# Performance work log

Measured on AMD Instinct MI355X. Metric: run time of the kernel, lower is better.

Reference implementation:

```python
import jax, jax.numpy as jnp
import numpy as np

N = 100000      # nodes
E = 1600000     # edges (avg degree 16)
F_N, F_E, H = 5, 3, 64
L = 3           # num GCN layers


def setup_inputs() -> dict:
    key = jax.random.key(0)
    ks = jax.random.split(key, 20)
    s = 0.05
    p = lambda k, shape: jax.random.normal(k, shape, jnp.float32) * s
    return {
        "x": jax.random.normal(ks[0], (N, F_N), jnp.float32),
        "edge_index": jax.random.randint(ks[1], (2, E), 0, N, dtype=jnp.int32),
        "edge_attr": jax.random.normal(ks[2], (E, F_E), jnp.float32),
        # node / edge encoders
        "Wn": p(ks[3], (F_N, H)), "bn": jnp.zeros((H,), jnp.float32),
        "We": p(ks[4], (F_E, H)), "be": jnp.zeros((H,), jnp.float32),
        # stacked GCNConv weights [L, H, H] and biases [L, H]
        "Wc": p(ks[5], (L, H, H)), "bc": jnp.zeros((L, H), jnp.float32),
        # demand forecast head
        "Wd1": p(ks[6], (H, H // 2)), "bd1": jnp.zeros((H // 2,), jnp.float32),
        "Wd2": p(ks[7], (H // 2, 1)), "bd2": jnp.zeros((1,), jnp.float32),
        # inventory optimizer head
        "Wi1": p(ks[8], (H, H // 2)), "bi1": jnp.zeros((H // 2,), jnp.float32),
        "Wi2": p(ks[9], (H // 2, 1)), "bi2": jnp.zeros((1,), jnp.float32),
    }


def reference(x, edge_index, edge_attr, Wn, bn, We, be, Wc, bc,
              Wd1, bd1, Wd2, bd2, Wi1, bi1, Wi2, bi2):
    src, dst = edge_index[0], edge_index[1]
    n = x.shape[0]

    h = jax.nn.relu(x @ Wn + bn)                      # [N, H]
    _ea = jax.nn.relu(edge_attr @ We + be)            # encoded edge feats (GCNConv ignores them)

    # GCN symmetric normalization with self-loops: deg[i] = in_degree(i) + 1
    ones_e = jnp.ones(src.shape[0], h.dtype)
    deg = jax.ops.segment_sum(ones_e, dst, num_segments=n) + 1.0
    dinv = jax.lax.rsqrt(deg)                         # [N]
    norm_e = dinv[src] * dinv[dst]                    # [E]
    norm_self = (dinv * dinv)[:, None]                # [N, 1]

    for l in range(Wc.shape[0]):
        hw = h @ Wc[l]                                # [N, H]
        msgs = norm_e[:, None] * hw[src]              # gather + scale, [E, H]
        agg = jax.ops.segment_sum(msgs, dst, num_segments=n) + norm_self * hw
        h = jax.nn.relu(agg + bc[l])

    demand = jax.nn.relu(h @ Wd1 + bd1) @ Wd2 + bd2   # [N, 1]
    inventory = jax.nn.relu(h @ Wi1 + bi1) @ Wi2 + bi2
    return demand, inventory
```

## Files before the change

### kernel.cpp

```cpp
#include <hip/hip_runtime.h>

#define H 64
#define FN 5
#define EPB 4096
#define BSHIFT 8
#define CAP2 4864

typedef _Float16 half4 __attribute__((ext_vector_type(4)));
typedef _Float16 half8 __attribute__((ext_vector_type(8)));
typedef float    float8v __attribute__((ext_vector_type(8)));

__global__ void k_bscatter2(const int* __restrict__ src, const int* __restrict__ dst,
                            int* __restrict__ lofs_t, int* __restrict__ bcounts,
                            int* __restrict__ binned, int nE, int nbB, int nbE) {
    __shared__ int lh[512], lpos[512], lcur[512], tmp[256];
    __shared__ int stage[EPB];
    int t = threadIdx.x;
    int e0 = blockIdx.x * EPB;
    int es[16], ed[16];
    lh[t] = 0; lh[t + 256] = 0;
    __syncthreads();
#pragma unroll
    for (int i = 0; i < 16; ++i) {
        int e = e0 + i * 256 + t;
        bool v = e < nE;
        es[i] = v ? src[e] : 0;
        ed[i] = v ? dst[e] : -1;
        if (v) atomicAdd(&lh[ed[i] >> BSHIFT], 1);
    }
    __syncthreads();
    int a0 = lh[2 * t], a1 = lh[2 * t + 1];
    tmp[t] = a0 + a1;
    __syncthreads();
    for (int s = 1; s < 256; s <<= 1) {
        int a = (t >= s) ? tmp[t - s] : 0;
        __syncthreads();
        tmp[t] += a;
        __syncthreads();
    }
    int ex = tmp[t] - (a0 + a1);
    lpos[2 * t] = ex;
    lpos[2 * t + 1] = ex + a0;
    __syncthreads();
    lcur[t] = lpos[t]; lcur[t + 256] = lpos[t + 256];
    for (int b = t; b <= nbB; b += 256) lofs_t[(size_t)b * nbE + blockIdx.x] = lpos[b];
    for (int b = t; b < nbB; b += 256) if (lh[b]) atomicAdd(&bcounts[b], lh[b]);
    __syncthreads();
#pragma unroll
    for (int i = 0; i < 16; ++i) {
        if (ed[i] >= 0) {
            int b = ed[i] >> BSHIFT;
            int p = atomicAdd(&lcur[b], 1);
            stage[p] = es[i] | ((ed[i] & 255) << 17);
        }
    }
    __syncthreads();
    int total = lpos[nbB];
    for (int j = t; j < total; j += 256) binned[e0 + j] = stage[j];
}

__global__ void k_bscan2(const int* __restrict__ bcounts, int* __restrict__ bbase, int nbB) {
    __shared__ int tmp[512];
    int t = threadIdx.x;
    int v = (t < nbB) ? bcounts[t] : 0;
    tmp[t] = v;
    __syncthreads();
    for (int s = 1; s < 512; s <<= 1) {
        int a = (t >= s) ? tmp[t - s] : 0;
        __syncthreads();
        tmp[t] += a;
        __syncthreads();
    }
    if (t < nbB) bbase[t + 1] = tmp[t];
    if (t == 0) bbase[0] = 0;
}

__global__ void k_bcsr2(const int* __restrict__ binned, const int* __restrict__ lofs_t,
                        const int* __restrict__ bbase, int* __restrict__ row_ptr,
                        int* __restrict__ csr_src, float* __restrict__ dinv,
                        int n, int nE, int nbE, int nbB) {
    __shared__ int start_s[512], roff[513], tmp[256];
    __shared__ int deg[256], st[256], cur[256];
    __shared__ int lbuf[CAP2];
    __shared__ int stage2[CAP2];
    int t = threadIdx.x;
    int B = blockIdx.x;
    int node0 = B << BSHIFT;
    int nn = min(256, n - node0);
    int s0i = 2 * t, s1i = 2 * t + 1;
    int a0 = 0, a1 = 0;
    if (s0i < nbE) {
        int o0 = lofs_t[B * nbE + s0i], o1 = lofs_t[(B + 1) * nbE + s0i];
        a0 = o1 - o0;
        start_s[s0i] = s0i * EPB + o0;
    } else start_s[s0i] = 0;
    if (s1i < nbE) {
        int o0 = lofs_t[B * nbE + s1i], o1 = lofs_t[(B + 1) * nbE + s1i];
        a1 = o1 - o0;
        start_s[s1i] = s1i * EPB + o0;
    } else start_s[s1i] = 0;
    tmp[t] = a0 + a1;
    __syncthreads();
    for (int s = 1; s < 256; s <<= 1) {
        int a = (t >= s) ? tmp[t - s] : 0;
        __syncthreads();
        tmp[t] += a;
        __syncthreads();
    }
    int ex = tmp[t] - (a0 + a1);
    roff[2 * t] = ex;
    roff[2 * t + 1] = ex + a0;
    if (t == 255) roff[512] = tmp[255];
    __syncthreads();
    int total = min(roff[512], CAP2);
    for (int i = t; i < total; i += 256) {
        int lo = 0, hi = 512;
        while (hi - lo > 1) {
            int mid = (lo + hi) >> 1;
            if (roff[mid] <= i) lo = mid; else hi = mid;
        }
        lbuf[i] = binned[start_s[lo] + (i - roff[lo])];
    }
    deg[t] = 0;
    __syncthreads();
    for (int i = t; i < total; i += 256) atomicAdd(&deg[(lbuf[i] >> 17) & 255], 1);
    __syncthreads();
    tmp[t] = deg[t];
    __syncthreads();
    for (int s = 1; s < 256; s <<= 1) {
        int a = (t >= s) ? tmp[t - s] : 0;
        __syncthreads();
        tmp[t] += a;
        __syncthreads();
    }
    st[t] = tmp[t] - deg[t];
    cur[t] = st[t];
    __syncthreads();
    int base = bbase[B];
    if (t < nn) {
        row_ptr[node0 + t] = base + st[t];
        dinv[node0 + t] = 1.0f / sqrtf((float)deg[t] + 1.0f);
    }
    if (B == 0 && t == 0) row_ptr[n] = nE;
    for (int i = t; i < total; i += 256) {
        int p0 = lbuf[i];
        int p = atomicAdd(&cur[(p0 >> 17) & 255], 1);
        int sv = p0 & 0x1FFFF;
        if (p < CAP2) stage2[p] = sv;
        else csr_src[base + p] = sv;
    }
    __syncthreads();
    for (int i = t; i < total; i += 256) csr_src[base + i] = stage2[i];
}

__global__ void k_enc(const float* __restrict__ x, const float* __restrict__ Wn,
                      const float* __restrict__ bn, const float* __restrict__ dinv,
                      _Float16* __restrict__ g0, int n) {
    int tid = blockIdx.x * 256 + threadIdx.x;
    int ch = threadIdx.x & 63;
    int node0 = (tid >> 6) * 4;
    if (node0 >= n) return;
    float wr[FN];
#pragma unroll
    for (int k = 0; k < FN; ++k) wr[k] = Wn[k * H + ch];
    float b = bn[ch];
#pragma unroll
    for (int j = 0; j < 4; ++j) {
        int node = node0 + j;
        if (node < n) {
            float acc = b;
#pragma unroll
            for (int k = 0; k < FN; ++k)
                acc += x[(size_t)node * FN + k] * wr[k];
            g0[(size_t)node * H + ch] = (_Float16)(fmaxf(acc, 0.f) * dinv[node]);
        }
    }
}

__global__ void k_layer(const _Float16* __restrict__ gin, const int* __restrict__ csr_src,
                        const int* __restrict__ row_ptr, const float* __restrict__ dinv,
                        const float* __restrict__ W, const float* __restrict__ bias,
                        _Float16* __restrict__ gout, float* __restrict__ hout,
                        int n, int last) {
    __shared__ float As[64 * 68];
    __shared__ int rp_s[65];
    __shared__ float dv_s[64];
    int t = threadIdx.x;
    int wave = t >> 6, lane = t & 63;
    int base = blockIdx.x * 64;
    if (t < 65) rp_s[t] = row_ptr[min(base + t, n)];
    if (t >= 128 && t < 192) {
        int nd = base + (t - 128);
        dv_s[t - 128] = (nd < n) ? dinv[nd] : 0.f;
    }
    __syncthreads();

    int c8 = (lane >> 3) * 8;
    int slot = lane & 7;
    for (int it = 0; it < 8; ++it) {
        int rA = it * 8 + wave, rB = rA + 4;
        int nodeA = base + rA, nodeB = base + rB;
        float8v accA = 0.f, accB = 0.f;
        int iA = rp_s[rA], eA = rp_s[rA + 1];
        int iB = rp_s[rB], eB = rp_s[rB + 1];
        int cA = (eA - iA) >> 3, cB = (eB - iB) >> 3;
        int xA = 0, xB = 0, txA = 0, txB = 0;
        int tbA = iA + (cA << 3), tbB = iB + (cB << 3);
        bool tvA = (tbA + slot < eA), tvB = (tbB + slot < eB);
        if (cA) xA = csr_src[iA + slot];
        if (cB) xB = csr_src[iB + slot];
        if (tvA) txA = csr_src[tbA + slot];
        if (tvB) txB = csr_src[tbB + slot];
        while (cA && cB) {
            half8 vA = *(const half8*)(gin + (size_t)xA * H + c8);
            half8 vB = *(const half8*)(gin + (size_t)xB * H + c8);
            iA += 8; iB += 8; --cA; --cB;
            if (cA) xA = csr_src[iA + slot];
            if (cB) xB = csr_src[iB + slot];
#pragma unroll
            for (int k = 0; k < 8; ++k) { accA[k] += (float)vA[k]; accB[k] += (float)vB[k]; }
        }
        while (cA) {
            half8 vA = *(const half8*)(gin + (size_t)xA * H + c8);
            iA += 8; --cA;
            if (cA) xA = csr_src[iA + slot];
#pragma unroll
            for (int k = 0; k < 8; ++k) accA[k] += (float)vA[k];
        }
        while (cB) {
            half8 vB = *(const half8*)(gin + (size_t)xB * H + c8);
            iB += 8; --cB;
            if (cB) xB = csr_src[iB + slot];
#pragma unroll
            for (int k = 0; k < 8; ++k) accB[k] += (float)vB[k];
        }
        if (tvA) {
            half8 vA = *(const half8*)(gin + (size_t)txA * H + c8);
#pragma unroll
            for (int k = 0; k < 8; ++k) accA[k] += (float)vA[k];
        }
        if (tvB) {
            half8 vB = *(const half8*)(gin + (size_t)txB * H + c8);
#pragma unroll
            for (int k = 0; k < 8; ++k) accB[k] += (float)vB[k];
        }
#pragma unroll
        for (int m = 1; m <= 4; m <<= 1) {
#pragma unroll
            for (int k = 0; k < 8; ++k) {
                accA[k] += __shfl_xor(accA[k], m, 64);
                accB[k] += __shfl_xor(accB[k], m, 64);
            }
        }
        if (slot == 0) {
            float oA[8], oB[8];
            if (nodeA < n) {
                half8 sA = *(const half8*)(gin + (size_t)nodeA * H + c8);
                float dA = dv_s[rA];
#pragma unroll
                for (int k = 0; k < 8; ++k) oA[k] = (accA[k] + (float)sA[k]) * dA;
            } else {
#pragma unroll
                for (int k = 0; k < 8; ++k) oA[k] = 0.f;
            }
            if (nodeB < n) {
                half8 sB = *(const half8*)(gin + (size_t)nodeB * H + c8);
                float dB = dv_s[rB];
#pragma unroll
                for (int k = 0; k < 8; ++k) oB[k] = (accB[k] + (float)sB[k]) * dB;
            } else {
#pragma unroll
                for (int k = 0; k < 8; ++k) oB[k] = 0.f;
            }
            *(float4*)&As[rA * 68 + c8]     = make_float4(oA[0], oA[1], oA[2], oA[3]);
            *(float4*)&As[rA * 68 + c8 + 4] = make_float4(oA[4], oA[5], oA[6], oA[7]);
            *(float4*)&As[rB * 68 + c8]     = make_float4(oB[0], oB[1], oB[2], oB[3]);
            *(float4*)&As[rB * 68 + c8 + 4] = make_float4(oB[4], oB[5], oB[6], oB[7]);
        }
    }
    __syncthreads();

    int tx = t & 15, ty = t >> 4;
    int c0 = tx * 4;
    const float* a0 = As + (ty * 4 + 0) * 68;
    const float* a1 = As + (ty * 4 + 1) * 68;
    const float* a2 = As + (ty * 4 + 2) * 68;
    const float* a3 = As + (ty * 4 + 3) * 68;
    float4 acc0 = make_float4(0.f, 0.f, 0.f, 0.f);
    float4 acc1 = acc0, acc2 = acc0, acc3 = acc0;
#pragma unroll 16
    for (int k = 0; k < H; ++k) {
        float4 w = *(const float4*)(W + k * H + c0);
        float v0 = a0[k], v1 = a1[k], v2 = a2[k], v3 = a3[k];
        acc0.x += v0 * w.x; acc0.y += v0 * w.y; acc0.z += v0 * w.z; acc0.w += v0 * w.w;
        acc1.x += v1 * w.x; acc1.y += v1 * w.y; acc1.z += v1 * w.z; acc1.w += v1 * w.w;
        acc2.x += v2 * w.x; acc2.y += v2 * w.y; acc2.z += v2 * w.z; acc2.w += v2 * w.w;
        acc3.x += v3 * w.x; acc3.y += v3 * w.y; acc3.z += v3 * w.z; acc3.w += v3 * w.w;
    }
    float4 b = *(const float4*)(bias + c0);
    float4 accs[4] = {acc0, acc1, acc2, acc3};
#pragma unroll
    for (int rr = 0; rr < 4; ++rr) {
        int r = ty * 4 + rr;
        int row = base + r;
        if (row < n) {
            float4 o;
            o.x = fmaxf(accs[rr].x + b.x, 0.f);
            o.y = fmaxf(accs[rr].y + b.y, 0.f);
            o.z = fmaxf(accs[rr].z + b.z, 0.f);
            o.w = fmaxf(accs[rr].w + b.w, 0.f);
            if (last) {
                *(float4*)(hout + (size_t)row * H + c0) = o;
            } else {
                float d = dv_s[r];
                half4 hh;
                hh.x = (_Float16)(o.x * d);
                hh.y = (_Float16)(o.y * d);
                hh.z = (_Float16)(o.z * d);
                hh.w = (_Float16)(o.w * d);
                *(half4*)(gout + (size_t)row * H + c0) = hh;
            }
        }
    }
}

__global__ void k_heads(const float* __restrict__ h,
                        const float* __restrict__ Wd1, const float* __restrict__ bd1,
                        const float* __restrict__ Wd2, const float* __restrict__ bd2,
                        const float* __restrict__ Wi1, const float* __restrict__ bi1,
                        const float* __restrict__ Wi2, const float* __restrict__ bi2,
                        float* __restrict__ out, int n) {
    __shared__ float hs[64 * 65];
    int lane = threadIdx.x;
    int base = blockIdx.x * 64;
    for (int r = 0; r < 64; ++r) {
        int row = base + r;
        hs[r * 65 + lane] = (row < n) ? h[(size_t)row * H + lane] : 0.f;
    }
    __syncthreads();

    float accd[32], acci[32];
#pragma unroll
    for (int j = 0; j < 32; ++j) { accd[j] = bd1[j]; acci[j] = bi1[j]; }
    for (int k = 0; k < H; ++k) {
        float hk = hs[lane * 65 + k];
#pragma unroll
        for (int j = 0; j < 32; ++j) {
            accd[j] += hk * Wd1[k * 32 + j];
            acci[j] += hk * Wi1[k * 32 + j];
        }
    }
    float demand = bd2[0], inventory = bi2[0];
#pragma unroll
    for (int j = 0; j < 32; ++j) {
        demand    += fmaxf(accd[j], 0.f) * Wd2[j];
        inventory += fmaxf(acci[j], 0.f) * Wi2[j];
    }
    int node = base + lane;
    if (node < n) {
        out[node] = demand;
        out[n + node] = inventory;
    }
}

extern "C" void kernel_launch(void* const* d_in, const int* in_sizes, int n_in,
                              void* d_out, int out_size, void* d_ws, size_t ws_size,
                              hipStream_t stream) {
    const float* x   = (const float*)d_in[0];
    const int*   ei  = (const int*)  d_in[1];
    const float* Wn  = (const float*)d_in[3];
    const float* bn  = (const float*)d_in[4];
    const float* Wc  = (const float*)d_in[7];
    const float* bc  = (const float*)d_in[8];
    const float* Wd1 = (const float*)d_in[9];
    const float* bd1 = (const float*)d_in[10];
    const float* Wd2 = (const float*)d_in[11];
    const float* bd2 = (const float*)d_in[12];
    const float* Wi1 = (const float*)d_in[13];
    const float* bi1 = (const float*)d_in[14];
    const float* Wi2 = (const float*)d_in[15];
    const float* bi2 = (const float*)d_in[16];

    const int n  = in_sizes[0] / FN;
    const int nE = in_sizes[1] / 2;
    const int* src = ei;
    const int* dst = ei + nE;

    const int nbE = (nE + EPB - 1) / EPB;
    const int nbB = (n + 255) >> BSHIFT;
    const int nbL = (n + 63) / 64;

    char* w = (char*)d_ws;
    int* binned    = (int*)w;   w += (size_t)nbE * EPB * 4;
    int* csr_src   = (int*)w;   w += (size_t)nE * 4;
    int* row_ptr   = (int*)w;   w += (size_t)(n + 4) * 4;
    float* dinv    = (float*)w; w += (size_t)n * 4;
    int* lofs      = (int*)w;   w += (size_t)(nbB + 1) * nbE * 4;
    int* bcounts   = (int*)w;   w += 512 * 4;
    int* bbase     = (int*)w;   w += 516 * 4;
    float* hbuf    = (float*)w; w += (size_t)n * H * 4;
    _Float16* gA   = (_Float16*)w; w += (size_t)n * H * 2;
    _Float16* gB   = (_Float16*)w; w += (size_t)n * H * 2;

    hipMemsetAsync(bcounts, 0, 512 * 4, stream);

    k_bscatter2<<<nbE, 256, 0, stream>>>(src, dst, lofs, bcounts, binned, nE, nbB, nbE);
    k_bscan2   <<<1,   512, 0, stream>>>(bcounts, bbase, nbB);
    k_bcsr2    <<<nbB, 256, 0, stream>>>(binned, lofs, bbase, row_ptr, csr_src,
                                         dinv, n, nE, nbE, nbB);

    k_enc<<<(n + 15) / 16, 256, 0, stream>>>(x, Wn, bn, dinv, gA, n);

    k_layer<<<nbL, 256, 0, stream>>>(gA, csr_src, row_ptr, dinv, Wc,
                                     bc, gB, hbuf, n, 0);
    k_layer<<<nbL, 256, 0, stream>>>(gB, csr_src, row_ptr, dinv, Wc + (size_t)H * H,
                                     bc + H, gA, hbuf, n, 0);
    k_layer<<<nbL, 256, 0, stream>>>(gA, csr_src, row_ptr, dinv, Wc + (size_t)2 * H * H,
                                     bc + 2 * H, gB, hbuf, n, 1);

    k_heads<<<(n + 63) / 64, 64, 0, stream>>>(hbuf, Wd1, bd1, Wd2, bd2,
                                              Wi1, bi1, Wi2, bi2, (float*)d_out, n);
}
```

Measured before the change: 378.7 us.

## Fold bucket scan and node encoder into the CSR build kernel

Removes the single-block bucket prefix-scan kernel and the separate node encoder kernel. Each CSR block now computes its own bucket base by scanning the preceding bucket counts, and after building its rows it encodes its 256 nodes directly using the locally computed degree inverse. This cuts two kernel launches and the dinv round-trip through global memory. In exchange every block does a redundant partial scan, and the encoder now runs one thread per node with strided half8 stores instead of the coalesced per-channel layout.

After: 384.3 us. About the same (+1.5%).

```diff
diff --git a/kernel.cpp b/kernel.cpp
--- a/kernel.cpp
+++ b/kernel.cpp
@@ -59,25 +59,11 @@
     for (int j = t; j < total; j += 256) binned[e0 + j] = stage[j];
 }
 
-__global__ void k_bscan2(const int* __restrict__ bcounts, int* __restrict__ bbase, int nbB) {
-    __shared__ int tmp[512];
-    int t = threadIdx.x;
-    int v = (t < nbB) ? bcounts[t] : 0;
-    tmp[t] = v;
-    __syncthreads();
-    for (int s = 1; s < 512; s <<= 1) {
-        int a = (t >= s) ? tmp[t - s] : 0;
-        __syncthreads();
-        tmp[t] += a;
-        __syncthreads();
-    }
-    if (t < nbB) bbase[t + 1] = tmp[t];
-    if (t == 0) bbase[0] = 0;
-}
-
 __global__ void k_bcsr2(const int* __restrict__ binned, const int* __restrict__ lofs_t,
-                        const int* __restrict__ bbase, int* __restrict__ row_ptr,
+                        const int* __restrict__ bcounts, int* __restrict__ row_ptr,
                         int* __restrict__ csr_src, float* __restrict__ dinv,
+                        const float* __restrict__ x, const float* __restrict__ Wn,
+                        const float* __restrict__ bn, _Float16* __restrict__ g0,
                         int n, int nE, int nbE, int nbB) {
     __shared__ int start_s[512], roff[513], tmp[256];
     __shared__ int deg[256], st[256], cur[256];
@@ -87,6 +73,22 @@
     int B = blockIdx.x;
     int node0 = B << BSHIFT;
     int nn = min(256, n - node0);
+
+    {
+        int v0 = (t < B) ? bcounts[t] : 0;
+        int v1 = (t + 256 < B) ? bcounts[t + 256] : 0;
+        tmp[t] = v0 + v1;
+    }
+    __syncthreads();
+    for (int s = 1; s < 256; s <<= 1) {
+        int a = (t >= s) ? tmp[t - s] : 0;
+        __syncthreads();
+        tmp[t] += a;
+        __syncthreads();
+    }
+    int base = tmp[255];
+    __syncthreads();
+
     int s0i = 2 * t, s1i = 2 * t + 1;
     int a0 = 0, a1 = 0;
     if (s0i < nbE) {
@@ -136,10 +138,10 @@
     st[t] = tmp[t] - deg[t];
     cur[t] = st[t];
     __syncthreads();
-    int base = bbase[B];
+    float dvv = 1.0f / sqrtf((float)deg[t] + 1.0f);
     if (t < nn) {
         row_ptr[node0 + t] = base + st[t];
-        dinv[node0 + t] = 1.0f / sqrtf((float)deg[t] + 1.0f);
+        dinv[node0 + t] = dvv;
     }
     if (B == 0 && t == 0) row_ptr[n] = nE;
     for (int i = t; i < total; i += 256) {
@@ -151,28 +153,24 @@
     }
     __syncthreads();
     for (int i = t; i < total; i += 256) csr_src[base + i] = stage2[i];
-}
-
-__global__ void k_enc(const float* __restrict__ x, const float* __restrict__ Wn,
-                      const float* __restrict__ bn, const float* __restrict__ dinv,
-                      _Float16* __restrict__ g0, int n) {
-    int tid = blockIdx.x * 256 + threadIdx.x;
-    int ch = threadIdx.x & 63;
-    int node0 = (tid >> 6) * 4;
-    if (node0 >= n) return;
-    float wr[FN];
-#pragma unroll
-    for (int k = 0; k < FN; ++k) wr[k] = Wn[k * H + ch];
-    float b = bn[ch];
-#pragma unroll
-    for (int j = 0; j < 4; ++j) {
-        int node = node0 + j;
-        if (node < n) {
-            float acc = b;
-#pragma unroll
-            for (int k = 0; k < FN; ++k)
-                acc += x[(size_t)node * FN + k] * wr[k];
-            g0[(size_t)node * H + ch] = (_Float16)(fmaxf(acc, 0.f) * dinv[node]);
+
+    if (t < nn) {
+        int node = node0 + t;
+        float xr[FN];
+#pragma unroll
+        for (int k = 0; k < FN; ++k) xr[k] = x[(size_t)node * FN + k];
+#pragma unroll
+        for (int c0 = 0; c0 < H; c0 += 8) {
+            half8 hh;
+#pragma unroll
+            for (int j = 0; j < 8; ++j) {
+                float acc = bn[c0 + j];
+#pragma unroll
+                for (int k = 0; k < FN; ++k)
+                    acc += xr[k] * Wn[k * H + c0 + j];
+                hh[j] = (_Float16)(fmaxf(acc, 0.f) * dvv);
+            }
+            *(half8*)(g0 + (size_t)node * H + c0) = hh;
         }
     }
 }
@@ -397,7 +395,6 @@
     float* dinv    = (float*)w; w += (size_t)n * 4;
     int* lofs      = (int*)w;   w += (size_t)(nbB + 1) * nbE * 4;
     int* bcounts   = (int*)w;   w += 512 * 4;
-    int* bbase     = (int*)w;   w += 516 * 4;
     float* hbuf    = (float*)w; w += (size_t)n * H * 4;
     _Float16* gA   = (_Float16*)w; w += (size_t)n * H * 2;
     _Float16* gB   = (_Float16*)w; w += (size_t)n * H * 2;
@@ -405,11 +402,8 @@
     hipMemsetAsync(bcounts, 0, 512 * 4, stream);
 
     k_bscatter2<<<nbE, 256, 0, stream>>>(src, dst, lofs, bcounts, binned, nE, nbB, nbE);
-    k_bscan2   <<<1,   512, 0, stream>>>(bcounts, bbase, nbB);
-    k_bcsr2    <<<nbB, 256, 0, stream>>>(binned, lofs, bbase, row_ptr, csr_src,
-                                         dinv, n, nE, nbE, nbB);
-
-    k_enc<<<(n + 15) / 16, 256, 0, stream>>>(x, Wn, bn, dinv, gA, n);
+    k_bcsr2    <<<nbB, 256, 0, stream>>>(binned, lofs, bcounts, row_ptr, csr_src,
+                                         dinv, x, Wn, bn, gA, n, nE, nbE, nbB);
 
     k_layer<<<nbL, 256, 0, stream>>>(gA, csr_src, row_ptr, dinv, Wc,
                                      bc, gB, hbuf, n, 0);
```
